# Optimization experiments

Measured on AMD Instinct MI355X. Metric: run time of the kernel, lower is better.

Reference implementation:

```python
import jax, jax.numpy as jnp
import numpy as np

B, S, D_MODEL, D_ATTN = 4, 2048, 1024, 1024
NEG_INF = jnp.float32(-jnp.inf)


def setup_inputs() -> dict:
    key = jax.random.key(0)
    ks = jax.random.split(key, 6)
    scale = 1.0 / np.sqrt(D_MODEL)
    return {
        "x": jax.random.normal(ks[0], (B, S, D_MODEL), dtype=jnp.float32),
        "mask": jnp.ones((B, S), dtype=jnp.float32),
        "Wq": jax.random.normal(ks[1], (D_ATTN, D_MODEL), dtype=jnp.float32) * scale,
        "Wk": jax.random.normal(ks[2], (D_ATTN, D_MODEL), dtype=jnp.float32) * scale,
        "Wv": jax.random.normal(ks[3], (D_ATTN, D_MODEL), dtype=jnp.float32) * scale,
        "Wo": jax.random.normal(ks[4], (D_MODEL, D_ATTN), dtype=jnp.float32) * scale,
        "bo": jnp.zeros((D_MODEL,), dtype=jnp.float32),
    }


def reference(x, mask, Wq, Wk, Wv, Wo, bo):
    # x: [B,S,Dm]; torch Linear weight is [out,in], so y = x @ W.T
    q = jnp.einsum("bsd,ad->bsa", x, Wq)  # [B,S,Da]
    k = jnp.einsum("bsd,ad->bsa", x, Wk)
    v = jnp.einsum("bsd,ad->bsa", x, Wv)  # NOTE: v from x (original quirk)
    logits = jnp.einsum("bqa,bka->bqk", q, k)  # [B,S,S]
    # causal mask (cross_attention=True path): keep lower triangle incl. diag
    causal = jnp.tril(jnp.ones((S, S), dtype=bool))
    logits = jnp.where(causal[None], logits, NEG_INF)
    # padding mask: outer product of per-token mask
    square_mask = mask[:, :, None] * mask[:, None, :]  # [B,S,S]
    logits = jnp.where(square_mask == 1, logits, NEG_INF)
    # scale by sqrt(d_model) AFTER masking (as in original)
    attn = jax.nn.softmax(logits / jnp.sqrt(jnp.float32(D_MODEL)), axis=-1)
    attn_out = jnp.einsum("bqk,bka->bqa", attn, v)  # [B,S,Da]
    return jnp.einsum("bsa,da->bsd", attn_out, Wo) + bo
```

## Files before the change

kernel.cpp:

```cpp
#include <hip/hip_runtime.h>
#include <hip/hip_bf16.h>
#include <cstdio>

typedef __bf16 bf16x8 __attribute__((ext_vector_type(8)));
typedef float f32x4 __attribute__((ext_vector_type(4)));

#define BM 128
#define BN 128
#define BK 64

__device__ __forceinline__ unsigned short f2bf(float f) {
  union { float f; unsigned u; } v; v.f = f;
  unsigned u = v.u;
  return (unsigned short)((u + 0x7FFFu + ((u >> 16) & 1u)) >> 16);
}

__device__ __forceinline__ float bf2f(unsigned short s) {
  union { unsigned u; float f; } v; v.u = ((unsigned)s) << 16;
  return v.f;
}

#define GLOAD16(gsrc, ldst) \
  __builtin_amdgcn_global_load_lds((const __attribute__((address_space(1))) void*)(gsrc), \
                                   (__attribute__((address_space(3))) void*)(ldst), 16, 0, 0)

#define SB_KLOOP(Ab, Bb)                                                        \
  for (int kt = 0; kt < 16; kt++) {                                             \
    const unsigned short* Ak = (Ab) + kt * BK;                                  \
    const unsigned short* Bk = (Bb) + kt * BK;                                  \
    _Pragma("unroll")                                                           \
    for (int r = 0; r < 4; r++) {                                               \
      int row = r * 32 + srow;                                                  \
      int sc = sch ^ (row & 7);                                                 \
      GLOAD16(Ak + (long)row * 1024 + sc * 8, &lds[0][(r * 32 + wave * 8) * BK]);\
    }                                                                           \
    _Pragma("unroll")                                                           \
    for (int r = 0; r < 4; r++) {                                               \
      int row = r * 32 + srow;                                                  \
      int sc = sch ^ (row & 7);                                                 \
      GLOAD16(Bk + (long)row * 1024 + sc * 8, &lds[1][(r * 32 + wave * 8) * BK]);\
    }                                                                           \
    __syncthreads();                                                            \
    _Pragma("unroll")                                                           \
    for (int s = 0; s < 2; s++) {                                               \
      bf16x8 av[4], bv[4];                                                      \
      _Pragma("unroll")                                                         \
      for (int i = 0; i < 4; i++) av[i] = *reinterpret_cast<const bf16x8*>(lds[0] + aOff[i][s]); \
      _Pragma("unroll")                                                         \
      for (int j = 0; j < 4; j++) bv[j] = *reinterpret_cast<const bf16x8*>(lds[1] + bOff[j][s]); \
      _Pragma("unroll")                                                         \
      for (int i = 0; i < 4; i++)                                               \
        _Pragma("unroll")                                                       \
        for (int j = 0; j < 4; j++)                                             \
          acc[i][j] = __builtin_amdgcn_mfma_f32_16x16x32_bf16(av[i], bv[j], acc[i][j], 0, 0, 0); \
    }                                                                           \
    __syncthreads();                                                            \
  }

#define SB_PREAMBLE                                                             \
  const int tid = threadIdx.x;                                                  \
  const int lane = tid & 63;                                                    \
  const int wave = tid >> 6;                                                    \
  const int wr = wave >> 1, wc = wave & 1;                                      \
  const int srow = tid >> 3;                                                    \
  const int sch = tid & 7;                                                      \
  const f32x4 fzero = {0.f, 0.f, 0.f, 0.f};                                     \
  f32x4 acc[4][4];                                                              \
  _Pragma("unroll")                                                             \
  for (int i = 0; i < 4; i++)                                                   \
    _Pragma("unroll")                                                           \
    for (int j = 0; j < 4; j++) acc[i][j] = fzero;                              \
  int aOff[4][2], bOff[4][2];                                                   \
  _Pragma("unroll")                                                             \
  for (int i = 0; i < 4; i++) {                                                 \
    _Pragma("unroll")                                                           \
    for (int s = 0; s < 2; s++) {                                               \
      int ra = wr * 64 + i * 16 + (lane & 15);                                  \
      aOff[i][s] = ra * BK + (((s * 4 + (lane >> 4)) ^ (ra & 7)) * 8);          \
      int rb = wc * 64 + i * 16 + (lane & 15);                                  \
      bOff[i][s] = rb * BK + (((s * 4 + (lane >> 4)) ^ (rb & 7)) * 8);          \
    }                                                                           \
  }

__global__ __launch_bounds__(256, 3)
void dispA(const unsigned short* __restrict__ Xbf, const unsigned short* __restrict__ Wqk,
           const unsigned short* __restrict__ Wob, const unsigned short* __restrict__ Wvt,
           unsigned short* __restrict__ Qb, unsigned short* __restrict__ Kb,
           unsigned short* __restrict__ Wvo)
{
  __shared__ short lds[2][BM * BK];
  const int flat = blockIdx.x;
  const bool isQK = flat < 1024;
  int m0, n0;
  const unsigned short *Ab, *Bb;
  if (isQK) {
    const int swz = (flat & 7) * 128 + (flat >> 3);
    const int bx = swz & 15, by = swz >> 4;
    m0 = by * BM; n0 = bx * BN;
    Ab = Xbf + (long)m0 * 1024;
    Bb = Wqk + (long)n0 * 1024;
  } else {
    const int t = flat - 1024;
    m0 = (t >> 3) * BM; n0 = (t & 7) * BN;
    Ab = Wob + (long)m0 * 1024;
    Bb = Wvt + (long)n0 * 1024;
  }

  SB_PREAMBLE
  SB_KLOOP(Ab, Bb)

  const int rb4 = (lane >> 4) * 4;
  const int cl = lane & 15;
#pragma unroll
  for (int i = 0; i < 4; i++) {
#pragma unroll
    for (int j = 0; j < 4; j++) {
      const int gm = m0 + wr * 64 + i * 16 + rb4;
      const int gn = n0 + wc * 64 + j * 16 + cl;
      if (isQK) {
        if (gn < 1024) {
#pragma unroll
          for (int r = 0; r < 4; r++)
            Qb[(long)(gm + r) * 1024 + gn] = f2bf(acc[i][j][r]);
        } else {
#pragma unroll
          for (int r = 0; r < 4; r++)
            Kb[(long)(gm + r) * 1024 + (gn - 1024)] = f2bf(acc[i][j][r]);
        }
      } else {
#pragma unroll
        for (int r = 0; r < 4; r++)
          Wvo[(long)(gm + r) * 1024 + gn] = f2bf(acc[i][j][r]);
      }
    }
  }
}

__global__ __launch_bounds__(256, 3)
void dispB(const unsigned short* __restrict__ Xbf, const unsigned short* __restrict__ Wvo,
           const unsigned short* __restrict__ Qb, const unsigned short* __restrict__ Kb,
           unsigned short* __restrict__ VWt, unsigned short* __restrict__ Sb)
{
  __shared__ short lds[2][BM * BK];
  const int flat = blockIdx.x;
  const bool isVW = flat < 512;
  int m0, n0, bz = 0;
  const unsigned short *Ab, *Bb;
  if (isVW) {
    const int swz = (flat & 7) * 64 + (flat >> 3);
    const int bx = swz & 7, by = swz >> 3;
    m0 = by * BM; n0 = bx * BN;
    Ab = Xbf + (long)m0 * 1024;
    Bb = Wvo + (long)n0 * 1024;
  } else {
    const int t = flat - 512;
    bz = t / 136;
    const int tt = t - bz * 136;
    const int swz = (tt & 7) * 17 + (tt >> 3);
    int i = (int)((sqrtf(8.f * (float)swz + 1.f) - 1.f) * 0.5f);
    while ((i + 1) * (i + 2) / 2 <= swz) ++i;
    while (i * (i + 1) / 2 > swz) --i;
    const int j = swz - i * (i + 1) / 2;
    m0 = i * BM; n0 = j * BN;
    Ab = Qb + ((long)bz * 2048 + m0) * 1024;
    Bb = Kb + ((long)bz * 2048 + n0) * 1024;
  }

  SB_PREAMBLE
  SB_KLOOP(Ab, Bb)

  const int rb4 = (lane >> 4) * 4;
  const int cl = lane & 15;
#pragma unroll
  for (int i = 0; i < 4; i++) {
#pragma unroll
    for (int j = 0; j < 4; j++) {
      const int gm = m0 + wr * 64 + i * 16 + rb4;
      const int gn = n0 + wc * 64 + j * 16 + cl;
      if (isVW) {
        const int b = gm >> 11;
        const int sIdx = gm & 2047;
        unsigned short* C = VWt + (long)b * (2048L * 1024) + (long)gn * 2048 + sIdx;
        ushort4 pk;
        pk.x = f2bf(acc[i][j][0]);
        pk.y = f2bf(acc[i][j][1]);
        pk.z = f2bf(acc[i][j][2]);
        pk.w = f2bf(acc[i][j][3]);
        *reinterpret_cast<ushort4*>(C) = pk;
      } else {
        unsigned short* C = Sb + (long)bz * (2048L * 2048);
#pragma unroll
        for (int r = 0; r < 4; r++)
          C[(long)(gm + r) * 2048 + gn] = f2bf(acc[i][j][r] * 0.03125f);
      }
    }
  }
}

__global__ __launch_bounds__(256, 2)
void gemm_pv(const unsigned short* __restrict__ A, const unsigned short* __restrict__ B,
             float* __restrict__ Cv, const float* __restrict__ bias,
             int K, int ldA, int ldB, int ldC,
             long aBat, long bBat, long cBat)
{
  const int gx = gridDim.x;
  const int nwg = gx * gridDim.y;
  const int flat = blockIdx.y * gx + blockIdx.x;
  const int qch = nwg >> 3, rch = nwg & 7;
  const int xcd = flat & 7, idx = flat >> 3;
  const int swz = (xcd < rch ? xcd * (qch + 1) : rch * (qch + 1) + (xcd - rch) * qch) + idx;
  const int bx = swz % gx;
  int by = swz / gx;
  by = gridDim.y - 1 - by;

  const int m0 = by * BM;
  const int n0 = bx * BN;
  const int bz = blockIdx.z;

  const unsigned short* Ab = A + (long)bz * aBat + (long)m0 * ldA;
  const unsigned short* Bb = B + (long)bz * bBat + (long)n0 * ldB;

  __shared__ short lds[2][2][BM * BK];

  const int tid = threadIdx.x;
  const int lane = tid & 63;
  const int wave = tid >> 6;
  const int wr = wave >> 1, wc = wave & 1;

  const int Keff = min(K, m0 + BM);
  const int nk = Keff / BK;

  const int srow = tid >> 3;
  const int sch = tid & 7;

  const f32x4 fzero = {0.f, 0.f, 0.f, 0.f};
  f32x4 acc[4][4];
#pragma unroll
  for (int i = 0; i < 4; i++)
#pragma unroll
    for (int j = 0; j < 4; j++) acc[i][j] = fzero;

  int aOff[4][2], bOff[4][2];
#pragma unroll
  for (int i = 0; i < 4; i++) {
#pragma unroll
    for (int s = 0; s < 2; s++) {
      int ra = wr * 64 + i * 16 + (lane & 15);
      aOff[i][s] = ra * BK + (((s * 4 + (lane >> 4)) ^ (ra & 7)) * 8);
      int rb = wc * 64 + i * 16 + (lane & 15);
      bOff[i][s] = rb * BK + (((s * 4 + (lane >> 4)) ^ (rb & 7)) * 8);
    }
  }

  auto stage = [&](int buf, int kt) {
    const unsigned short* Ak = Ab + kt * BK;
    const unsigned short* Bk = Bb + kt * BK;
#pragma unroll
    for (int r = 0; r < 4; r++) {
      int row = r * 32 + srow;
      int sc = sch ^ (row & 7);
      GLOAD16(Ak + (long)row * ldA + sc * 8, &lds[buf][0][(r * 32 + wave * 8) * BK]);
    }
#pragma unroll
    for (int r = 0; r < 4; r++) {
      int row = r * 32 + srow;
      int sc = sch ^ (row & 7);
      GLOAD16(Bk + (long)row * ldB + sc * 8, &lds[buf][1][(r * 32 + wave * 8) * BK]);
    }
  };

  stage(0, 0);
  stage(1, 1);
  asm volatile("s_waitcnt vmcnt(8)" ::: "memory");
  __builtin_amdgcn_sched_barrier(0);
  __builtin_amdgcn_s_barrier();

  int cur = 0;
  for (int kt = 0; kt < nk; kt++) {
    const short* La = lds[cur][0];
    const short* Lb = lds[cur][1];
    bf16x8 av[2][4], bv[2][4];
#pragma unroll
    for (int s = 0; s < 2; s++) {
#pragma unroll
      for (int i = 0; i < 4; i++) {
        av[s][i] = *reinterpret_cast<const bf16x8*>(La + aOff[i][s]);
        bv[s][i] = *reinterpret_cast<const bf16x8*>(Lb + bOff[i][s]);
      }
    }
    asm volatile("s_waitcnt lgkmcnt(0)" ::: "memory");
    __builtin_amdgcn_sched_barrier(0);
    __builtin_amdgcn_s_barrier();
    __builtin_amdgcn_sched_barrier(0);

    if (kt + 2 < nk) {
      stage(cur, kt + 2);
      asm volatile("s_waitcnt vmcnt(8)" ::: "memory");
    } else if (kt + 1 < nk) {
      asm volatile("s_waitcnt vmcnt(0)" ::: "memory");
    }
    if (kt + 1 < nk) {
      __builtin_amdgcn_s_barrier();
      __builtin_amdgcn_sched_barrier(0);
    }

    __builtin_amdgcn_s_setprio(1);
#pragma unroll
    for (int s = 0; s < 2; s++)
#pragma unroll
      for (int i = 0; i < 4; i++)
#pragma unroll
        for (int j = 0; j < 4; j++)
          acc[i][j] = __builtin_amdgcn_mfma_f32_16x16x32_bf16(av[s][i], bv[s][j], acc[i][j], 0, 0, 0);
    __builtin_amdgcn_s_setprio(0);
    __builtin_amdgcn_sched_barrier(0);
    cur ^= 1;
  }

  const int rb4 = (lane >> 4) * 4;
  const int cl = lane & 15;
#pragma unroll
  for (int i = 0; i < 4; i++) {
#pragma unroll
    for (int j = 0; j < 4; j++) {
      const int gm = m0 + wr * 64 + i * 16 + rb4;
      const int gn = n0 + wc * 64 + j * 16 + cl;
      float* C = Cv + (long)bz * cBat;
      const float bb = bias[gn];
#pragma unroll
      for (int r = 0; r < 4; r++)
        C[(long)(gm + r) * ldC + gn] = acc[i][j][r] + bb;
    }
  }
}

__global__ __launch_bounds__(256)
void softmax_rows(const unsigned short* __restrict__ Sb, const float* __restrict__ maskv,
                  unsigned short* __restrict__ P, int Sdim)
{
  const int wv = threadIdx.x >> 6;
  const int lane = threadIdx.x & 63;
  const int q = blockIdx.x * 4 + wv;
  const int b = blockIdx.y;
  const int kmax = (q & ~127) + 128;
  const unsigned short* row = Sb + ((long)b * Sdim + q) * Sdim;
  unsigned short* prow = P + ((long)b * Sdim + q) * Sdim;
  const float* mrow = maskv + (long)b * Sdim;
  const float mq = mrow[q];

  float v[4][8];
  float mx = -INFINITY;
#pragma unroll
  for (int c = 0; c < 4; c++) {
    const int k0 = c * 512 + lane * 8;
    if (c * 512 < kmax) {
      uint4 raw = *reinterpret_cast<const uint4*>(row + k0);
      const unsigned short* us = reinterpret_cast<const unsigned short*>(&raw);
      float4 ma = *reinterpret_cast<const float4*>(mrow + k0);
      float4 mb = *reinterpret_cast<const float4*>(mrow + k0 + 4);
      float mv[8] = {ma.x, ma.y, ma.z, ma.w, mb.x, mb.y, mb.z, mb.w};
#pragma unroll
      for (int u = 0; u < 8; u++) {
        const int k = k0 + u;
        const bool ok = (k <= q) && (mq * mv[u] == 1.0f);
        v[c][u] = ok ? bf2f(us[u]) : -INFINITY;
        mx = fmaxf(mx, v[c][u]);
      }
    } else {
#pragma unroll
      for (int u = 0; u < 8; u++) v[c][u] = -INFINITY;
    }
  }
#pragma unroll
  for (int o = 32; o; o >>= 1) mx = fmaxf(mx, __shfl_xor(mx, o));

  float sm = 0.f;
#pragma unroll
  for (int c = 0; c < 4; c++)
#pragma unroll
    for (int u = 0; u < 8; u++) {
      v[c][u] = (v[c][u] > -INFINITY) ? __expf(v[c][u] - mx) : 0.f;
      sm += v[c][u];
    }
#pragma unroll
  for (int o = 32; o; o >>= 1) sm += __shfl_xor(sm, o);
  const float inv = 1.0f / sm;

#pragma unroll
  for (int c = 0; c < 4; c++) {
    if (c * 512 < kmax) {
      union { unsigned short us[8]; uint4 u4; } pk;
#pragma unroll
      for (int u = 0; u < 8; u++) pk.us[u] = f2bf(v[c][u] * inv);
      *reinterpret_cast<uint4*>(prow + c * 512 + lane * 8) = pk.u4;
    }
  }
}

__global__ __launch_bounds__(256)
void cast_all2(const float* __restrict__ x, const float* __restrict__ Wq,
               const float* __restrict__ Wk, const float* __restrict__ Wv,
               const float* __restrict__ Wo,
               unsigned short* __restrict__ xb, unsigned short* __restrict__ Wqk,
               unsigned short* __restrict__ Wob, unsigned short* __restrict__ Wvt)
{
  __shared__ float t[64][65];
  const int blk = blockIdx.x;
  const int tid = threadIdx.x;
  if (blk < 5632) {
    const float* src;
    unsigned short* dst;
    int i;
    if (blk < 4096) {
      src = x; dst = xb; i = (blk * 256 + tid) * 8;
    } else {
      const int w = (blk - 4096) >> 9;
      const int off = (blk - 4096) & 511;
      src = (w == 0) ? Wq : (w == 1) ? Wk : Wo;
      dst = (w == 0) ? Wqk : (w == 1) ? (Wqk + 1024L * 1024) : Wob;
      i = (off * 256 + tid) * 8;
    }
    float4 a = *reinterpret_cast<const float4*>(src + i);
    float4 b = *reinterpret_cast<const float4*>(src + i + 4);
    union { unsigned short us[8]; uint4 u4; } pk;
    pk.us[0] = f2bf(a.x); pk.us[1] = f2bf(a.y); pk.us[2] = f2bf(a.z); pk.us[3] = f2bf(a.w);
    pk.us[4] = f2bf(b.x); pk.us[5] = f2bf(b.y); pk.us[6] = f2bf(b.z); pk.us[7] = f2bf(b.w);
    *reinterpret_cast<uint4*>(dst + i) = pk.u4;
    return;
  }
  const int tile = blk - 5632;
  const int a0 = (tile >> 4) * 64;
  const int m0 = (tile & 15) * 64;
#pragma unroll
  for (int i = 0; i < 4; i++) {
    const int row = (tid >> 4) + i * 16;
    const int col4 = tid & 15;
    float4 f4 = *reinterpret_cast<const float4*>(Wv + (long)(a0 + row) * 1024 + m0 + col4 * 4);
    t[row][col4 * 4 + 0] = f4.x;
    t[row][col4 * 4 + 1] = f4.y;
    t[row][col4 * 4 + 2] = f4.z;
    t[row][col4 * 4 + 3] = f4.w;
  }
  __syncthreads();
#pragma unroll
  for (int j = 0; j < 2; j++) {
    const int mm = (tid >> 3) + j * 32;
    const int aa0 = (tid & 7) * 8;
    union { unsigned short us[8]; uint4 u4; } pk;
#pragma unroll
    for (int u = 0; u < 8; u++) pk.us[u] = f2bf(t[aa0 + u][mm]);
    *reinterpret_cast<uint4*>(Wvt + (long)(m0 + mm) * 1024 + a0 + aa0) = pk.u4;
  }
}

extern "C" void kernel_launch(void* const* d_in, const int* in_sizes, int n_in,
                              void* d_out, int out_size, void* d_ws, size_t ws_size,
                              hipStream_t stream)
{
  const int B = 4, S = 2048, D = 1024;
  const float* x  = (const float*)d_in[0];
  const float* mk = (const float*)d_in[1];
  const float* Wq = (const float*)d_in[2];
  const float* Wk = (const float*)d_in[3];
  const float* Wv = (const float*)d_in[4];
  const float* Wo = (const float*)d_in[5];
  const float* bo = (const float*)d_in[6];
  float* out = (float*)d_out;

  char* ws = (char*)d_ws;
  const long MB = 1024L * 1024L;
  unsigned short* Xbf  = (unsigned short*)(ws + 0);
  unsigned short* Qb   = (unsigned short*)(ws + 16 * MB);
  unsigned short* Kb   = (unsigned short*)(ws + 32 * MB);
  unsigned short* VWt  = (unsigned short*)(ws + 48 * MB);
  unsigned short* Wqk  = (unsigned short*)(ws + 64 * MB);
  unsigned short* Wvo  = (unsigned short*)(ws + 68 * MB);
  unsigned short* Wob  = (unsigned short*)(ws + 70 * MB);
  unsigned short* Sbuf = (unsigned short*)(ws + 72 * MB);
  unsigned short* Wvt  = Sbuf;
  unsigned short* P    = Qb;

  if (ws_size < (size_t)(104 * MB)) {
    fprintf(stderr, "kernel_launch: ws too small (%zu bytes, need 104MB)\n", ws_size);
    return;
  }

  cast_all2<<<dim3(5888), dim3(256), 0, stream>>>(x, Wq, Wk, Wv, Wo, Xbf, Wqk, Wob, Wvt);
  dispA<<<dim3(1088), dim3(256), 0, stream>>>(Xbf, Wqk, Wob, Wvt, Qb, Kb, Wvo);
  dispB<<<dim3(1056), dim3(256), 0, stream>>>(Xbf, Wvo, Qb, Kb, VWt, Sbuf);
  softmax_rows<<<dim3(512, 4), dim3(256), 0, stream>>>(Sbuf, mk, P, 2048);
  dim3 gO(1024 / BN, 2048 / BM, 4);
  gemm_pv<<<gO, dim3(256), 0, stream>>>(P, VWt, out, bo,
                                        2048, 2048, 2048, 1024,
                                        (long)S * S, (long)D * S, (long)S * D);
}
```

Baseline: 163.4 us.

## Reorder launch stages so Wo·Wv product overlaps x cast and VW joins QK GEMM

Splits the cast kernel into a weight-only cast, then a prep kernel that computes the small Wo·Wv^T GEMM while the remaining blocks cast x to bf16. The V·Wvo GEMM moves into the same dispatch as the Q/K projection, and the causal Q·K^T score GEMM becomes its own kernel. The aim is to balance work across launches and hide the small GEMM behind the bandwidth-bound cast, at the cost of one extra kernel launch. gemm_pv now reverses the row order only for batches 2 and 3.

```diff
diff --git a/kernel.cpp b/kernel.cpp
--- a/kernel.cpp
+++ b/kernel.cpp
@@ -82,11 +82,99 @@
     }                                                                           \
   }
 
+__global__ __launch_bounds__(256)
+void cast_w(const float* __restrict__ Wq, const float* __restrict__ Wk,
+            const float* __restrict__ Wv, const float* __restrict__ Wo,
+            unsigned short* __restrict__ Wqk, unsigned short* __restrict__ Wob,
+            unsigned short* __restrict__ Wvt)
+{
+  const int blk = blockIdx.x;
+  const int tid = threadIdx.x;
+  if (blk < 1536) {
+    const int w = blk >> 9;
+    const int off = blk & 511;
+    const float* src = (w == 0) ? Wq : (w == 1) ? Wk : Wo;
+    unsigned short* dst = (w == 0) ? Wqk : (w == 1) ? (Wqk + 1024L * 1024) : Wob;
+    const int i = (off * 256 + tid) * 8;
+    float4 a = *reinterpret_cast<const float4*>(src + i);
+    float4 b = *reinterpret_cast<const float4*>(src + i + 4);
+    union { unsigned short us[8]; uint4 u4; } pk;
+    pk.us[0] = f2bf(a.x); pk.us[1] = f2bf(a.y); pk.us[2] = f2bf(a.z); pk.us[3] = f2bf(a.w);
+    pk.us[4] = f2bf(b.x); pk.us[5] = f2bf(b.y); pk.us[6] = f2bf(b.z); pk.us[7] = f2bf(b.w);
+    *reinterpret_cast<uint4*>(dst + i) = pk.u4;
+    return;
+  }
+  __shared__ float t[64][65];
+  const int tile = blk - 1536;
+  const int a0 = (tile >> 4) * 64;
+  const int m0 = (tile & 15) * 64;
+#pragma unroll
+  for (int i = 0; i < 4; i++) {
+    const int row = (tid >> 4) + i * 16;
+    const int col4 = tid & 15;
+    float4 f4 = *reinterpret_cast<const float4*>(Wv + (long)(a0 + row) * 1024 + m0 + col4 * 4);
+    t[row][col4 * 4 + 0] = f4.x;
+    t[row][col4 * 4 + 1] = f4.y;
+    t[row][col4 * 4 + 2] = f4.z;
+    t[row][col4 * 4 + 3] = f4.w;
+  }
+  __syncthreads();
+#pragma unroll
+  for (int j = 0; j < 2; j++) {
+    const int mm = (tid >> 3) + j * 32;
+    const int aa0 = (tid & 7) * 8;
+    union { unsigned short us[8]; uint4 u4; } pk;
+#pragma unroll
+    for (int u = 0; u < 8; u++) pk.us[u] = f2bf(t[aa0 + u][mm]);
+    *reinterpret_cast<uint4*>(Wvt + (long)(m0 + mm) * 1024 + a0 + aa0) = pk.u4;
+  }
+}
+
 __global__ __launch_bounds__(256, 3)
-void dispA(const unsigned short* __restrict__ Xbf, const unsigned short* __restrict__ Wqk,
+void prep2(const float* __restrict__ x, unsigned short* __restrict__ xb,
            const unsigned short* __restrict__ Wob, const unsigned short* __restrict__ Wvt,
-           unsigned short* __restrict__ Qb, unsigned short* __restrict__ Kb,
            unsigned short* __restrict__ Wvo)
+{
+  __shared__ short lds[2][BM * BK];
+  if (blockIdx.x >= 64) {
+    const int blk = blockIdx.x - 64;
+    const int i = (blk * 256 + (int)threadIdx.x) * 8;
+    float4 a = *reinterpret_cast<const float4*>(x + i);
+    float4 b = *reinterpret_cast<const float4*>(x + i + 4);
+    union { unsigned short us[8]; uint4 u4; } pk;
+    pk.us[0] = f2bf(a.x); pk.us[1] = f2bf(a.y); pk.us[2] = f2bf(a.z); pk.us[3] = f2bf(a.w);
+    pk.us[4] = f2bf(b.x); pk.us[5] = f2bf(b.y); pk.us[6] = f2bf(b.z); pk.us[7] = f2bf(b.w);
+    *reinterpret_cast<uint4*>(xb + i) = pk.u4;
+    return;
+  }
+  const int t = blockIdx.x;
+  const int m0 = (t >> 3) * BM, n0 = (t & 7) * BN;
+  const unsigned short* Ab = Wob + (long)m0 * 1024;
+  const unsigned short* Bb = Wvt + (long)n0 * 1024;
+
+  SB_PREAMBLE
+  SB_KLOOP(Ab, Bb)
+
+  const int rb4 = (lane >> 4) * 4;
+  const int cl = lane & 15;
+#pragma unroll
+  for (int i = 0; i < 4; i++) {
+#pragma unroll
+    for (int j = 0; j < 4; j++) {
+      const int gm = m0 + wr * 64 + i * 16 + rb4;
+      const int gn = n0 + wc * 64 + j * 16 + cl;
+#pragma unroll
+      for (int r = 0; r < 4; r++)
+        Wvo[(long)(gm + r) * 1024 + gn] = f2bf(acc[i][j][r]);
+    }
+  }
+}
+
+__global__ __launch_bounds__(256, 3)
+void dispA2(const unsigned short* __restrict__ Xbf, const unsigned short* __restrict__ Wqk,
+            const unsigned short* __restrict__ Wvo,
+            unsigned short* __restrict__ Qb, unsigned short* __restrict__ Kb,
+            unsigned short* __restrict__ VWt)
 {
   __shared__ short lds[2][BM * BK];
   const int flat = blockIdx.x;
@@ -101,9 +189,11 @@
     Bb = Wqk + (long)n0 * 1024;
   } else {
     const int t = flat - 1024;
-    m0 = (t >> 3) * BM; n0 = (t & 7) * BN;
-    Ab = Wob + (long)m0 * 1024;
-    Bb = Wvt + (long)n0 * 1024;
+    const int swz = (t & 7) * 64 + (t >> 3);
+    const int bx = swz & 7, by = swz >> 3;
+    m0 = by * BM; n0 = bx * BN;
+    Ab = Xbf + (long)m0 * 1024;
+    Bb = Wvo + (long)n0 * 1024;
   }
 
   SB_PREAMBLE
@@ -128,56 +218,6 @@
             Kb[(long)(gm + r) * 1024 + (gn - 1024)] = f2bf(acc[i][j][r]);
         }
       } else {
-#pragma unroll
-        for (int r = 0; r < 4; r++)
-          Wvo[(long)(gm + r) * 1024 + gn] = f2bf(acc[i][j][r]);
-      }
-    }
-  }
-}
-
-__global__ __launch_bounds__(256, 3)
-void dispB(const unsigned short* __restrict__ Xbf, const unsigned short* __restrict__ Wvo,
-           const unsigned short* __restrict__ Qb, const unsigned short* __restrict__ Kb,
-           unsigned short* __restrict__ VWt, unsigned short* __restrict__ Sb)
-{
-  __shared__ short lds[2][BM * BK];
-  const int flat = blockIdx.x;
-  const bool isVW = flat < 512;
-  int m0, n0, bz = 0;
-  const unsigned short *Ab, *Bb;
-  if (isVW) {
-    const int swz = (flat & 7) * 64 + (flat >> 3);
-    const int bx = swz & 7, by = swz >> 3;
-    m0 = by * BM; n0 = bx * BN;
-    Ab = Xbf + (long)m0 * 1024;
-    Bb = Wvo + (long)n0 * 1024;
-  } else {
-    const int t = flat - 512;
-    bz = t / 136;
-    const int tt = t - bz * 136;
-    const int swz = (tt & 7) * 17 + (tt >> 3);
-    int i = (int)((sqrtf(8.f * (float)swz + 1.f) - 1.f) * 0.5f);
-    while ((i + 1) * (i + 2) / 2 <= swz) ++i;
-    while (i * (i + 1) / 2 > swz) --i;
-    const int j = swz - i * (i + 1) / 2;
-    m0 = i * BM; n0 = j * BN;
-    Ab = Qb + ((long)bz * 2048 + m0) * 1024;
-    Bb = Kb + ((long)bz * 2048 + n0) * 1024;
-  }
-
-  SB_PREAMBLE
-  SB_KLOOP(Ab, Bb)
-
-  const int rb4 = (lane >> 4) * 4;
-  const int cl = lane & 15;
-#pragma unroll
-  for (int i = 0; i < 4; i++) {
-#pragma unroll
-    for (int j = 0; j < 4; j++) {
-      const int gm = m0 + wr * 64 + i * 16 + rb4;
-      const int gn = n0 + wc * 64 + j * 16 + cl;
-      if (isVW) {
         const int b = gm >> 11;
         const int sIdx = gm & 2047;
         unsigned short* C = VWt + (long)b * (2048L * 1024) + (long)gn * 2048 + sIdx;
@@ -187,12 +227,43 @@
         pk.z = f2bf(acc[i][j][2]);
         pk.w = f2bf(acc[i][j][3]);
         *reinterpret_cast<ushort4*>(C) = pk;
-      } else {
-        unsigned short* C = Sb + (long)bz * (2048L * 2048);
-#pragma unroll
-        for (int r = 0; r < 4; r++)
-          C[(long)(gm + r) * 2048 + gn] = f2bf(acc[i][j][r] * 0.03125f);
       }
+    }
+  }
+}
+
+__global__ __launch_bounds__(256, 3)
+void dispS(const unsigned short* __restrict__ Qb, const unsigned short* __restrict__ Kb,
+           unsigned short* __restrict__ Sb)
+{
+  __shared__ short lds[2][BM * BK];
+  const int t = blockIdx.x;
+  const int bz = t / 136;
+  const int tt = t - bz * 136;
+  const int swz = (tt & 7) * 17 + (tt >> 3);
+  int i = (int)((sqrtf(8.f * (float)swz + 1.f) - 1.f) * 0.5f);
+  while ((i + 1) * (i + 2) / 2 <= swz) ++i;
+  while (i * (i + 1) / 2 > swz) --i;
+  const int j = swz - i * (i + 1) / 2;
+  const int m0 = i * BM, n0 = j * BN;
+  const unsigned short* Ab = Qb + ((long)bz * 2048 + m0) * 1024;
+  const unsigned short* Bb = Kb + ((long)bz * 2048 + n0) * 1024;
+
+  SB_PREAMBLE
+  SB_KLOOP(Ab, Bb)
+
+  const int rb4 = (lane >> 4) * 4;
+  const int cl = lane & 15;
+  unsigned short* C = Sb + (long)bz * (2048L * 2048);
+#pragma unroll
+  for (int ii = 0; ii < 4; ii++) {
+#pragma unroll
+    for (int jj = 0; jj < 4; jj++) {
+      const int gm = m0 + wr * 64 + ii * 16 + rb4;
+      const int gn = n0 + wc * 64 + jj * 16 + cl;
+#pragma unroll
+      for (int r = 0; r < 4; r++)
+        C[(long)(gm + r) * 2048 + gn] = f2bf(acc[ii][jj][r] * 0.03125f);
     }
   }
 }
@@ -210,12 +281,12 @@
   const int xcd = flat & 7, idx = flat >> 3;
   const int swz = (xcd < rch ? xcd * (qch + 1) : rch * (qch + 1) + (xcd - rch) * qch) + idx;
   const int bx = swz % gx;
+  const int bz = blockIdx.z;
   int by = swz / gx;
-  by = gridDim.y - 1 - by;
+  if (bz >= 2) by = gridDim.y - 1 - by;
 
   const int m0 = by * BM;
   const int n0 = bx * BN;
-  const int bz = blockIdx.z;
 
   const unsigned short* Ab = A + (long)bz * aBat + (long)m0 * ldA;
   const unsigned short* Bb = B + (long)bz * bBat + (long)n0 * ldB;
@@ -394,62 +465,6 @@
       for (int u = 0; u < 8; u++) pk.us[u] = f2bf(v[c][u] * inv);
       *reinterpret_cast<uint4*>(prow + c * 512 + lane * 8) = pk.u4;
     }
-  }
-}
-
-__global__ __launch_bounds__(256)
-void cast_all2(const float* __restrict__ x, const float* __restrict__ Wq,
-               const float* __restrict__ Wk, const float* __restrict__ Wv,
-               const float* __restrict__ Wo,
-               unsigned short* __restrict__ xb, unsigned short* __restrict__ Wqk,
-               unsigned short* __restrict__ Wob, unsigned short* __restrict__ Wvt)
-{
-  __shared__ float t[64][65];
-  const int blk = blockIdx.x;
-  const int tid = threadIdx.x;
-  if (blk < 5632) {
-    const float* src;
-    unsigned short* dst;
-    int i;
-    if (blk < 4096) {
-      src = x; dst = xb; i = (blk * 256 + tid) * 8;
-    } else {
-      const int w = (blk - 4096) >> 9;
-      const int off = (blk - 4096) & 511;
-      src = (w == 0) ? Wq : (w == 1) ? Wk : Wo;
-      dst = (w == 0) ? Wqk : (w == 1) ? (Wqk + 1024L * 1024) : Wob;
-      i = (off * 256 + tid) * 8;
-    }
-    float4 a = *reinterpret_cast<const float4*>(src + i);
-    float4 b = *reinterpret_cast<const float4*>(src + i + 4);
-    union { unsigned short us[8]; uint4 u4; } pk;
-    pk.us[0] = f2bf(a.x); pk.us[1] = f2bf(a.y); pk.us[2] = f2bf(a.z); pk.us[3] = f2bf(a.w);
-    pk.us[4] = f2bf(b.x); pk.us[5] = f2bf(b.y); pk.us[6] = f2bf(b.z); pk.us[7] = f2bf(b.w);
-    *reinterpret_cast<uint4*>(dst + i) = pk.u4;
-    return;
-  }
-  const int tile = blk - 5632;
-  const int a0 = (tile >> 4) * 64;
-  const int m0 = (tile & 15) * 64;
-#pragma unroll
-  for (int i = 0; i < 4; i++) {
-    const int row = (tid >> 4) + i * 16;
-    const int col4 = tid & 15;
-    float4 f4 = *reinterpret_cast<const float4*>(Wv + (long)(a0 + row) * 1024 + m0 + col4 * 4);
-    t[row][col4 * 4 + 0] = f4.x;
-    t[row][col4 * 4 + 1] = f4.y;
-    t[row][col4 * 4 + 2] = f4.z;
-    t[row][col4 * 4 + 3] = f4.w;
-  }
-  __syncthreads();
-#pragma unroll
-  for (int j = 0; j < 2; j++) {
-    const int mm = (tid >> 3) + j * 32;
-    const int aa0 = (tid & 7) * 8;
-    union { unsigned short us[8]; uint4 u4; } pk;
-#pragma unroll
-    for (int u = 0; u < 8; u++) pk.us[u] = f2bf(t[aa0 + u][mm]);
-    *reinterpret_cast<uint4*>(Wvt + (long)(m0 + mm) * 1024 + a0 + aa0) = pk.u4;
   }
 }
 
@@ -485,9 +500,10 @@
     return;
   }
 
-  cast_all2<<<dim3(5888), dim3(256), 0, stream>>>(x, Wq, Wk, Wv, Wo, Xbf, Wqk, Wob, Wvt);
-  dispA<<<dim3(1088), dim3(256), 0, stream>>>(Xbf, Wqk, Wob, Wvt, Qb, Kb, Wvo);
-  dispB<<<dim3(1056), dim3(256), 0, stream>>>(Xbf, Wvo, Qb, Kb, VWt, Sbuf);
+  cast_w<<<dim3(1792), dim3(256), 0, stream>>>(Wq, Wk, Wv, Wo, Wqk, Wob, Wvt);
+  prep2<<<dim3(4160), dim3(256), 0, stream>>>(x, Xbf, Wob, Wvt, Wvo);
+  dispA2<<<dim3(1536), dim3(256), 0, stream>>>(Xbf, Wqk, Wvo, Qb, Kb, VWt);
+  dispS<<<dim3(544), dim3(256), 0, stream>>>(Qb, Kb, Sbuf);
   softmax_rows<<<dim3(512, 4), dim3(256), 0, stream>>>(Sbuf, mk, P, 2048);
   dim3 gO(1024 / BN, 2048 / BM, 4);
   gemm_pv<<<gO, dim3(256), 0, stream>>>(P, VWt, out, bo,
```

Result: faster. 155.7 us (-4.7%).
